# Kernel optimization log

Measured on AMD Instinct MI355X. Metric: run time of the kernel, lower is better.

The kernel has to match this reference:

```python
import jax, jax.numpy as jnp
import numpy as np

TWO_PI = 2.0 * np.pi

def _round_ste(y):
    # forward: round(y); backward: identity (straight-through), matching _RoundSTE
    return y + jax.lax.stop_gradient(jnp.round(y) - y)

def _anti_wrap(x):
    return jnp.abs(x - _round_ste(x / TWO_PI) * TWO_PI)

def setup_inputs() -> dict:
    key = jax.random.key(0)
    k1, k2 = jax.random.split(key)
    B, F, T = 32, 513, 1600  # F = n_fft//2 + 1 with n_fft=1024
    phase_r = jax.random.normal(k1, (B, F, T), dtype=jnp.float32)
    phase_g = jax.random.normal(k2, (B, F, T), dtype=jnp.float32)
    return {"phase_r": phase_r, "phase_g": phase_g}

def reference(phase_r, phase_g):
    # d[b,f,t] = phase_r - phase_g
    d = phase_r - phase_g
    ip_loss = jnp.mean(_anti_wrap(d))

    # GD_matrix has -1 on diag, +1 on superdiag; matmul(phase^T, M)[b,t,f]
    # = phase[b,f-1,t] - phase[b,f,t] (with implicit zero at f=-1).
    # GD_r - GD_g is the same banded diff applied to d along freq axis.
    d_shift_f = jnp.pad(d, ((0, 0), (1, 0), (0, 0)))[:, :-1, :]  # d[b,f-1,t], 0 at f=0
    gd_loss = jnp.mean(_anti_wrap(d_shift_f - d))

    # PTD_matrix: same banded diff along time axis.
    d_shift_t = jnp.pad(d, ((0, 0), (0, 0), (1, 0)))[:, :, :-1]  # d[b,f,t-1], 0 at t=0
    ptd_loss = jnp.mean(_anti_wrap(d_shift_t - d))

    return (ip_loss, gd_loss, ptd_loss)
```

## Files before the change

kernel.cpp:

```cpp
#include <hip/hip_runtime.h>
#include <math.h>

constexpr int Bc = 32, Fc = 513, Tc = 1600;
constexpr int BLK = 128;
constexpr int VEC = 4;
constexpr int TT  = BLK * VEC;
constexpr int NTT = (Tc + TT - 1) / TT;
constexpr int FCH = 27;
constexpr int NFC = (Fc + FCH - 1) / FCH;
constexpr int NBLK = Bc * NFC * NTT;
constexpr long long NTOT = (long long)Bc * Fc * Tc;

__device__ __forceinline__ float anti_wrap_f(float x) {
    float r = rintf(x * 0.15915494309189535f);
    return fabsf(fmaf(-r, 6.283185307179586f, x));
}

__device__ __forceinline__ void block_reduce3(float& a, float& b, float& c) {
    #pragma unroll
    for (int off = 32; off > 0; off >>= 1) {
        a += __shfl_down(a, off);
        b += __shfl_down(b, off);
        c += __shfl_down(c, off);
    }
    __shared__ float sm[3][BLK / 64];
    const int lane = threadIdx.x & 63, wid = threadIdx.x >> 6;
    if (lane == 0) { sm[0][wid] = a; sm[1][wid] = b; sm[2][wid] = c; }
    __syncthreads();
    if (threadIdx.x == 0) {
        a = sm[0][0]; b = sm[1][0]; c = sm[2][0];
        #pragma unroll
        for (int w = 1; w < BLK / 64; ++w) {
            a += sm[0][w]; b += sm[1][w]; c += sm[2][w];
        }
    }
}

__global__ __launch_bounds__(BLK) void phase_main(
        const float* __restrict__ pr, const float* __restrict__ pg,
        float* __restrict__ partials,
        float* __restrict__ out,
        int use_atomic)
{
    const int tile = blockIdx.x;
    const int fc   = blockIdx.y;
    const int b    = blockIdx.z;
    const int t0   = tile * TT + (int)threadIdx.x * VEC;
    const int f0   = fc * FCH;
    const int f1   = min(f0 + FCH, Fc);

    float s_ip = 0.f, s_gd = 0.f, s_ptd = 0.f;

    if (t0 < Tc) {
        const size_t baseb = (size_t)b * Fc * Tc + (size_t)t0;
        float4 pd;
        if (f0 == 0) {
            pd = make_float4(0.f, 0.f, 0.f, 0.f);
        } else {
            const float* ap = pr + baseb + (size_t)(f0 - 1) * Tc;
            const float* gp = pg + baseb + (size_t)(f0 - 1) * Tc;
            float4 a = *(const float4*)ap;
            float4 g = *(const float4*)gp;
            pd = make_float4(a.x - g.x, a.y - g.y, a.z - g.z, a.w - g.w);
        }
        for (int f = f0; f < f1; ++f) {
            const float* ap = pr + baseb + (size_t)f * Tc;
            const float* gp = pg + baseb + (size_t)f * Tc;
            float4 a = *(const float4*)ap;
            float4 g = *(const float4*)gp;
            float dm1 = 0.f;
            if (t0 > 0) dm1 = ap[-1] - gp[-1];
            float4 d = make_float4(a.x - g.x, a.y - g.y, a.z - g.z, a.w - g.w);

            s_ip  += anti_wrap_f(d.x) + anti_wrap_f(d.y)
                   + anti_wrap_f(d.z) + anti_wrap_f(d.w);
            s_gd  += anti_wrap_f(pd.x - d.x) + anti_wrap_f(pd.y - d.y)
                   + anti_wrap_f(pd.z - d.z) + anti_wrap_f(pd.w - d.w);
            s_ptd += anti_wrap_f(dm1 - d.x) + anti_wrap_f(d.x - d.y)
                   + anti_wrap_f(d.y - d.z) + anti_wrap_f(d.z - d.w);
            pd = d;
        }
    }

    block_reduce3(s_ip, s_gd, s_ptd);

    if (threadIdx.x == 0) {
        if (use_atomic) {
            const float invN = (float)(1.0 / (double)NTOT);
            atomicAdd(out + 0, s_ip * invN);
            atomicAdd(out + 1, s_gd * invN);
            atomicAdd(out + 2, s_ptd * invN);
        } else {
            const int bid = (blockIdx.z * gridDim.y + blockIdx.y) * gridDim.x
                          + blockIdx.x;
            partials[0 * NBLK + bid] = s_ip;
            partials[1 * NBLK + bid] = s_gd;
            partials[2 * NBLK + bid] = s_ptd;
        }
    }
}

__global__ __launch_bounds__(256) void phase_reduce(
        const float* __restrict__ partials, float* __restrict__ out)
{
    __shared__ float sm[4];
    const int tid = threadIdx.x;
    const int lane = tid & 63, wid = tid >> 6;
    for (int c = 0; c < 3; ++c) {
        float s = 0.f;
        for (int i = tid; i < NBLK; i += 256) s += partials[c * NBLK + i];
        #pragma unroll
        for (int off = 32; off > 0; off >>= 1) s += __shfl_down(s, off);
        __syncthreads();
        if (lane == 0) sm[wid] = s;
        __syncthreads();
        if (tid == 0) {
            float t = sm[0] + sm[1] + sm[2] + sm[3];
            out[c] = t * (float)(1.0 / (double)NTOT);
        }
    }
}

__global__ void zero3(float* out) {
    if (threadIdx.x < 3) out[threadIdx.x] = 0.f;
}

extern "C" void kernel_launch(void* const* d_in, const int* in_sizes, int n_in,
                              void* d_out, int out_size, void* d_ws, size_t ws_size,
                              hipStream_t stream) {
    const float* pr = (const float*)d_in[0];
    const float* pg = (const float*)d_in[1];
    float* out = (float*)d_out;
    dim3 grid(NTT, NFC, Bc);

    if (ws_size >= (size_t)NBLK * 3 * sizeof(float)) {
        float* partials = (float*)d_ws;
        phase_main<<<grid, BLK, 0, stream>>>(pr, pg, partials, nullptr, 0);
        phase_reduce<<<1, 256, 0, stream>>>(partials, out);
    } else {
        zero3<<<1, 64, 0, stream>>>(out);
        phase_main<<<grid, BLK, 0, stream>>>(pr, pg, nullptr, out, 1);
    }
}
```

Baseline: 49.74 us.

## Prefetch next frequency row, shrink frequency chunk, parallelize final reduction

The main loop now software-pipelines its loads, fetching the next frequency row's float4 and neighbour scalars while the current row's anti-wrap math runs. This hides global memory latency. The frequency chunk per block shrinks from 27 to 9, which triples the block count to raise parallelism but re-reads one extra halo row per chunk. The final reduction uses three blocks, one per loss term, instead of one block looping over all three.

```diff
diff --git a/kernel.cpp b/kernel.cpp
--- a/kernel.cpp
+++ b/kernel.cpp
@@ -6,7 +6,7 @@
 constexpr int VEC = 4;
 constexpr int TT  = BLK * VEC;
 constexpr int NTT = (Tc + TT - 1) / TT;
-constexpr int FCH = 27;
+constexpr int FCH = 9;
 constexpr int NFC = (Fc + FCH - 1) / FCH;
 constexpr int NBLK = Bc * NFC * NTT;
 constexpr long long NTOT = (long long)Bc * Fc * Tc;
@@ -53,23 +53,36 @@
 
     if (t0 < Tc) {
         const size_t baseb = (size_t)b * Fc * Tc + (size_t)t0;
+        const float* ap = pr + baseb + (size_t)f0 * Tc;
+        const float* gp = pg + baseb + (size_t)f0 * Tc;
+
         float4 pd;
         if (f0 == 0) {
             pd = make_float4(0.f, 0.f, 0.f, 0.f);
         } else {
-            const float* ap = pr + baseb + (size_t)(f0 - 1) * Tc;
-            const float* gp = pg + baseb + (size_t)(f0 - 1) * Tc;
-            float4 a = *(const float4*)ap;
-            float4 g = *(const float4*)gp;
+            float4 a = *(const float4*)(ap - Tc);
+            float4 g = *(const float4*)(gp - Tc);
             pd = make_float4(a.x - g.x, a.y - g.y, a.z - g.z, a.w - g.w);
         }
+
+        float4 a = *(const float4*)ap;
+        float4 g = *(const float4*)gp;
+        float am1 = 0.f, gm1 = 0.f;
+        if (t0 > 0) { am1 = ap[-1]; gm1 = gp[-1]; }
+
         for (int f = f0; f < f1; ++f) {
-            const float* ap = pr + baseb + (size_t)f * Tc;
-            const float* gp = pg + baseb + (size_t)f * Tc;
-            float4 a = *(const float4*)ap;
-            float4 g = *(const float4*)gp;
-            float dm1 = 0.f;
-            if (t0 > 0) dm1 = ap[-1] - gp[-1];
+            const float* apn = ap + Tc;
+            const float* gpn = gp + Tc;
+            float4 an = make_float4(0.f, 0.f, 0.f, 0.f);
+            float4 gn = make_float4(0.f, 0.f, 0.f, 0.f);
+            float am1n = 0.f, gm1n = 0.f;
+            if (f + 1 < f1) {
+                an = *(const float4*)apn;
+                gn = *(const float4*)gpn;
+                if (t0 > 0) { am1n = apn[-1]; gm1n = gpn[-1]; }
+            }
+
+            float  dm1 = am1 - gm1;
             float4 d = make_float4(a.x - g.x, a.y - g.y, a.z - g.z, a.w - g.w);
 
             s_ip  += anti_wrap_f(d.x) + anti_wrap_f(d.y)
@@ -78,7 +91,10 @@
                    + anti_wrap_f(pd.z - d.z) + anti_wrap_f(pd.w - d.w);
             s_ptd += anti_wrap_f(dm1 - d.x) + anti_wrap_f(d.x - d.y)
                    + anti_wrap_f(d.y - d.z) + anti_wrap_f(d.z - d.w);
+
             pd = d;
+            a = an; g = gn; am1 = am1n; gm1 = gm1n;
+            ap = apn; gp = gpn;
         }
     }
 
@@ -103,21 +119,19 @@
 __global__ __launch_bounds__(256) void phase_reduce(
         const float* __restrict__ partials, float* __restrict__ out)
 {
+    const int c = blockIdx.x;
+    const int tid = threadIdx.x;
+    float s = 0.f;
+    for (int i = tid; i < NBLK; i += 256) s += partials[(size_t)c * NBLK + i];
+    #pragma unroll
+    for (int off = 32; off > 0; off >>= 1) s += __shfl_down(s, off);
     __shared__ float sm[4];
-    const int tid = threadIdx.x;
     const int lane = tid & 63, wid = tid >> 6;
-    for (int c = 0; c < 3; ++c) {
-        float s = 0.f;
-        for (int i = tid; i < NBLK; i += 256) s += partials[c * NBLK + i];
-        #pragma unroll
-        for (int off = 32; off > 0; off >>= 1) s += __shfl_down(s, off);
-        __syncthreads();
-        if (lane == 0) sm[wid] = s;
-        __syncthreads();
-        if (tid == 0) {
-            float t = sm[0] + sm[1] + sm[2] + sm[3];
-            out[c] = t * (float)(1.0 / (double)NTOT);
-        }
+    if (lane == 0) sm[wid] = s;
+    __syncthreads();
+    if (tid == 0) {
+        float t = sm[0] + sm[1] + sm[2] + sm[3];
+        out[c] = t * (float)(1.0 / (double)NTOT);
     }
 }
 
@@ -136,7 +150,7 @@
     if (ws_size >= (size_t)NBLK * 3 * sizeof(float)) {
         float* partials = (float*)d_ws;
         phase_main<<<grid, BLK, 0, stream>>>(pr, pg, partials, nullptr, 0);
-        phase_reduce<<<1, 256, 0, stream>>>(partials, out);
+        phase_reduce<<<3, 256, 0, stream>>>(partials, out);
     } else {
         zero3<<<1, 64, 0, stream>>>(out);
         phase_main<<<grid, BLK, 0, stream>>>(pr, pg, nullptr, out, 1);
```

After: 52.55 us. 5.7% more time.
